# Performance work log

Measured on AMD Instinct MI355X. Metric: run time of the kernel, lower is better.

The kernel has to match this reference:

```python
import jax, jax.numpy as jnp
import numpy as np

HEADS = 4
DIM_HEAD = 32
GROUPS = 32  # min(256//4, 32)
EPS = 1e-5


def setup_inputs() -> dict:
    key = jax.random.key(0)
    ks = jax.random.split(key, 5)
    B, C, H, W = 16, 256, 64, 64
    CD, HC, WC = 512, 32, 32
    hid = HEADS * DIM_HEAD  # 128
    return {
        "x": jax.random.normal(ks[0], (B, C, H, W), jnp.float32),
        "cond": jax.random.normal(ks[1], (B, CD, HC, WC), jnp.float32),
        "gn_w": jnp.ones((C,), jnp.float32),
        "gn_b": jnp.zeros((C,), jnp.float32),
        "w_q": jax.random.normal(ks[2], (hid, C), jnp.float32) * 0.05,
        "b_q": jnp.zeros((hid,), jnp.float32),
        "w_kv": jax.random.normal(ks[3], (2 * hid, CD), jnp.float32) * 0.05,
        "b_kv": jnp.zeros((2 * hid,), jnp.float32),
        "w_out": jax.random.normal(ks[4], (C, hid), jnp.float32) * 0.05,
        "b_out": jnp.zeros((C,), jnp.float32),
    }


def _group_norm(x, w, b):
    # x: (B, C, H, W); normalize per group over (channels-in-group, H, W)
    B, C, H, W = x.shape
    xg = x.reshape(B, GROUPS, C // GROUPS, H, W)
    mu = jnp.mean(xg, axis=(2, 3, 4), keepdims=True)
    var = jnp.var(xg, axis=(2, 3, 4), keepdims=True)
    xn = ((xg - mu) * jax.lax.rsqrt(var + EPS)).reshape(B, C, H, W)
    return xn * w[None, :, None, None] + b[None, :, None, None]


def _conv1x1(x, w, b):
    # x: (B, Cin, H, W), w: (Cout, Cin), b: (Cout,)
    return jnp.einsum('oc,bchw->bohw', w, x) + b[None, :, None, None]


def reference(x, cond, gn_w, gn_b, w_q, b_q, w_kv, b_kv, w_out, b_out):
    B, C, H, W = x.shape
    hid = HEADS * DIM_HEAD
    xn = _group_norm(x, gn_w, gn_b)
    q = _conv1x1(xn, w_q, b_q)          # (B, hid, H, W)
    kv = _conv1x1(cond, w_kv, b_kv)     # (B, 2*hid, Hc, Wc)
    Nc = kv.shape[2] * kv.shape[3]
    N = H * W
    k = kv[:, :hid].reshape(B, HEADS, DIM_HEAD, Nc)
    v = kv[:, hid:].reshape(B, HEADS, DIM_HEAD, Nc)
    q = q.reshape(B, HEADS, DIM_HEAD, N)
    k = jax.nn.softmax(k, axis=-1)
    # kv outer product: (B, heads, d, e)
    context = jnp.einsum('bhdn,bhen->bhde', k, v)
    # query contraction over d: (B, heads, e, n)
    out = jnp.einsum('bhde,bhdn->bhen', context, q)
    out = out.reshape(B, hid, H, W)
    return _conv1x1(out, w_out, b_out)
```

## Files before the change

kernel.cpp:

```cpp
#include <hip/hip_runtime.h>
#include <hip/hip_bf16.h>

typedef __attribute__((ext_vector_type(8))) short bf16x8;
typedef __attribute__((ext_vector_type(4))) float f32x4;

__device__ __forceinline__ ushort f2bf(float f) {
    __hip_bfloat16 h = __float2bfloat16(f);
    return __builtin_bit_cast(ushort, h);
}
__device__ __forceinline__ unsigned pack2(float a, float b) {
    return (unsigned)f2bf(a) | ((unsigned)f2bf(b) << 16);
}
__device__ __forceinline__ float bflo(unsigned u) { return __uint_as_float(u << 16); }
__device__ __forceinline__ float bfhi(unsigned u) { return __uint_as_float(u & 0xffff0000u); }

__device__ __forceinline__ void unpack8(uint4 r, float* o) {
    o[0] = bflo(r.x); o[1] = bfhi(r.x); o[2] = bflo(r.y); o[3] = bfhi(r.y);
    o[4] = bflo(r.z); o[5] = bfhi(r.z); o[6] = bflo(r.w); o[7] = bfhi(r.w);
}

__global__ __launch_bounds__(256) void kvprep_kernel(const float* __restrict__ w_kv,
                                                     const float* __restrict__ cond,
                                                     const float* __restrict__ b_kv,
                                                     ushort* __restrict__ kv16,
                                                     const float* __restrict__ x,
                                                     float* __restrict__ statacc,
                                                     float* __restrict__ zbase) {
    __shared__ ushort lA[128 * 64];
    __shared__ ushort lB[64 * 64];
    __shared__ float scratch[64 * 64];
    __shared__ float red[8];
    int bid = blockIdx.x, t = threadIdx.x;
    if (bid < 512) {
        int nb = bid & 15, ob = (bid >> 4) & 1, b = bid >> 5;
        int col0 = nb * 64, row0 = ob * 128;
        int l = t & 63, wid = t >> 6;
        int wr = wid >> 1, wc = wid & 1;
        int lr = l & 15, lg = l >> 4;
        const float* Ab32 = w_kv + (size_t)row0 * 512;
        const float* Bb = cond + (size_t)b * 512 * 1024 + col0;
        int sp = t & 31, sj = t >> 5;
        int rA = t >> 3, gAr = t & 7, gw = gAr ^ (rA & 7);
        int rB = t >> 4, gB = t & 15;
        float4 ka0_, ka1_, ka2_, ka3_, ka4_, ka5_, ka6_, ka7_;
        float4 kb0_, kb1_, kb2_, kb3_;
#define KP_LOADA(k0) { \
    ka0_ = *(const float4*)&Ab32[(size_t)(rA)      * 512 + (k0) + gAr * 8]; \
    ka1_ = *(const float4*)&Ab32[(size_t)(rA)      * 512 + (k0) + gAr * 8 + 4]; \
    ka2_ = *(const float4*)&Ab32[(size_t)(32 + rA) * 512 + (k0) + gAr * 8]; \
    ka3_ = *(const float4*)&Ab32[(size_t)(32 + rA) * 512 + (k0) + gAr * 8 + 4]; \
    ka4_ = *(const float4*)&Ab32[(size_t)(64 + rA) * 512 + (k0) + gAr * 8]; \
    ka5_ = *(const float4*)&Ab32[(size_t)(64 + rA) * 512 + (k0) + gAr * 8 + 4]; \
    ka6_ = *(const float4*)&Ab32[(size_t)(96 + rA) * 512 + (k0) + gAr * 8]; \
    ka7_ = *(const float4*)&Ab32[(size_t)(96 + rA) * 512 + (k0) + gAr * 8 + 4]; }
#define KP_LOADB(k0) { \
    kb0_ = *(const float4*)&Bb[(size_t)((k0) + rB)      * 1024 + gB * 4]; \
    kb1_ = *(const float4*)&Bb[(size_t)((k0) + 16 + rB) * 1024 + gB * 4]; \
    kb2_ = *(const float4*)&Bb[(size_t)((k0) + 32 + rB) * 1024 + gB * 4]; \
    kb3_ = *(const float4*)&Bb[(size_t)((k0) + 48 + rB) * 1024 + gB * 4]; }
#define KP_WRITEA() { \
    uint4 p; \
    p.x = pack2(ka0_.x, ka0_.y); p.y = pack2(ka0_.z, ka0_.w); \
    p.z = pack2(ka1_.x, ka1_.y); p.w = pack2(ka1_.z, ka1_.w); \
    *(uint4*)((char*)lA + (size_t)((rA)      * 8 + gw) * 16) = p; \
    p.x = pack2(ka2_.x, ka2_.y); p.y = pack2(ka2_.z, ka2_.w); \
    p.z = pack2(ka3_.x, ka3_.y); p.w = pack2(ka3_.z, ka3_.w); \
    *(uint4*)((char*)lA + (size_t)((32 + rA) * 8 + gw) * 16) = p; \
    p.x = pack2(ka4_.x, ka4_.y); p.y = pack2(ka4_.z, ka4_.w); \
    p.z = pack2(ka5_.x, ka5_.y); p.w = pack2(ka5_.z, ka5_.w); \
    *(uint4*)((char*)lA + (size_t)((64 + rA) * 8 + gw) * 16) = p; \
    p.x = pack2(ka6_.x, ka6_.y); p.y = pack2(ka6_.z, ka6_.w); \
    p.z = pack2(ka7_.x, ka7_.y); p.w = pack2(ka7_.z, ka7_.w); \
    *(uint4*)((char*)lA + (size_t)((96 + rA) * 8 + gw) * 16) = p; }
#define KP_WRITEB() { \
    *(float4*)((char*)scratch + (rB)      * 256 + (gB ^ (((rB)      >> 1) & 15)) * 16) = kb0_; \
    *(float4*)((char*)scratch + (16 + rB) * 256 + (gB ^ (((16 + rB) >> 1) & 15)) * 16) = kb1_; \
    *(float4*)((char*)scratch + (32 + rB) * 256 + (gB ^ (((32 + rB) >> 1) & 15)) * 16) = kb2_; \
    *(float4*)((char*)scratch + (48 + rB) * 256 + (gB ^ (((48 + rB) >> 1) & 15)) * 16) = kb3_; }
#define KP_PACKB() { \
    int swz = sp & 15; \
    float4 s0 = *(const float4*)((char*)scratch + (2*sp)   * 256 + ((2*sj)   ^ swz) * 16); \
    float4 s1 = *(const float4*)((char*)scratch + (2*sp)   * 256 + ((2*sj+1) ^ swz) * 16); \
    float4 s2 = *(const float4*)((char*)scratch + (2*sp+1) * 256 + ((2*sj)   ^ swz) * 16); \
    float4 s3 = *(const float4*)((char*)scratch + (2*sp+1) * 256 + ((2*sj+1) ^ swz) * 16); \
    float c0v[8] = {s0.x, s0.y, s0.z, s0.w, s1.x, s1.y, s1.z, s1.w}; \
    float c1v[8] = {s2.x, s2.y, s2.z, s2.w, s3.x, s3.y, s3.z, s3.w}; \
    _Pragma("unroll") \
    for (int w = 0; w < 8; ++w) { \
        int n = sj * 8 + w; \
        unsigned pk = pack2(c0v[w], c1v[w]); \
        *(unsigned*)((char*)lB + n * 128 + (((sp >> 2) ^ (n & 7)) * 16) + (sp & 3) * 4) = pk; \
    } }
        KP_LOADA(0); KP_LOADB(0);
        f32x4 acc[4][2] = {};
        for (int it = 0; it < 8; ++it) {
            KP_WRITEA();
            KP_WRITEB();
            __syncthreads();
            if (it < 7) { KP_LOADA(it * 64 + 64); KP_LOADB(it * 64 + 64); }
            KP_PACKB();
            __syncthreads();
            #pragma unroll
            for (int ks = 0; ks < 2; ++ks) {
                bf16x8 av[4], bv[2];
                #pragma unroll
                for (int mi = 0; mi < 4; ++mi) {
                    int ar = wr * 64 + mi * 16 + lr;
                    int q = (ks * 4 + lg) ^ (ar & 7);
                    av[mi] = *(const bf16x8*)((const char*)lA + ar * 128 + q * 16);
                }
                #pragma unroll
                for (int ni = 0; ni < 2; ++ni) {
                    int br = wc * 32 + ni * 16 + lr;
                    int q = (ks * 4 + lg) ^ (br & 7);
                    bv[ni] = *(const bf16x8*)((const char*)lB + br * 128 + q * 16);
                }
                #pragma unroll
                for (int mi = 0; mi < 4; ++mi)
                    #pragma unroll
                    for (int ni = 0; ni < 2; ++ni)
                        acc[mi][ni] = __builtin_amdgcn_mfma_f32_16x16x32_bf16(
                            av[mi], bv[ni], acc[mi][ni], 0, 0, 0);
            }
            __syncthreads();
        }
#undef KP_LOADA
#undef KP_LOADB
#undef KP_WRITEA
#undef KP_WRITEB
#undef KP_PACKB
        int orow = row0 + wr * 64, ocol = col0 + wc * 32 + lr;
        #pragma unroll
        for (int mi = 0; mi < 4; ++mi) {
            int rb = orow + mi * 16 + lg * 4;
            float4 b4 = *(const float4*)&b_kv[rb];
            float bvr[4] = {b4.x, b4.y, b4.z, b4.w};
            #pragma unroll
            for (int ni = 0; ni < 2; ++ni) {
                int cc = ocol + ni * 16;
                #pragma unroll
                for (int r = 0; r < 4; ++r)
                    kv16[((size_t)b * 256 + rb + r) * 1024 + cc] = f2bf(acc[mi][ni][r] + bvr[r]);
            }
        }
    } else {
        int bg = bid - 512;
        int zi = bg * 256 + t;
        if (zi < 67584) zbase[zi] = 0.f;
        const float4* xp = (const float4*)(x + (size_t)bg * 32768);
        float s = 0.f, ss = 0.f;
        #pragma unroll
        for (int j = 0; j < 32; ++j) {
            float4 v = xp[t + 256 * j];
            s  += v.x + v.y + v.z + v.w;
            ss += v.x*v.x + v.y*v.y + v.z*v.z + v.w*v.w;
        }
        #pragma unroll
        for (int off = 32; off > 0; off >>= 1) {
            s  += __shfl_down(s, off, 64);
            ss += __shfl_down(ss, off, 64);
        }
        int wave = t >> 6;
        if ((t & 63) == 0) { red[wave * 2] = s; red[wave * 2 + 1] = ss; }
        __syncthreads();
        if (t == 0) {
            statacc[bg * 2]     = red[0] + red[2] + red[4] + red[6];
            statacc[bg * 2 + 1] = red[1] + red[3] + red[5] + red[7];
        }
    }
}

__global__ __launch_bounds__(256) void ctx_partial_kernel(const ushort* __restrict__ kv,
                                                          float* __restrict__ rowsum,
                                                          float* __restrict__ ctx) {
    int bh = blockIdx.y, b = bh >> 2, h = bh & 3;
    int n0 = blockIdx.x * 128;
    __shared__ float pl[32][129], vl[32][129];
    int t = threadIdx.x;
    int r = t >> 3, cs = (t & 7) * 16;
    const ushort* kp = kv + ((size_t)b * 256 + h * 32 + r) * 1024 + n0 + cs;
    const ushort* vp = kv + ((size_t)b * 256 + 128 + h * 32 + r) * 1024 + n0 + cs;
    float kvals[16], vvals[16];
    unpack8(((const uint4*)kp)[0], kvals);
    unpack8(((const uint4*)kp)[1], kvals + 8);
    unpack8(((const uint4*)vp)[0], vvals);
    unpack8(((const uint4*)vp)[1], vvals + 8);
    float psum = 0.f;
    #pragma unroll
    for (int i = 0; i < 16; ++i) {
        float e = __expf(kvals[i]);
        pl[r][cs + i] = e;
        vl[r][cs + i] = vvals[i];
        psum += e;
    }
    psum += __shfl_xor(psum, 1, 64);
    psum += __shfl_xor(psum, 2, 64);
    psum += __shfl_xor(psum, 4, 64);
    if ((t & 7) == 0) atomicAdd(&rowsum[bh * 32 + r], psum);
    __syncthreads();
    int d0 = t >> 5, e0 = t & 31;
    float acc[4] = {0.f, 0.f, 0.f, 0.f};
    #pragma unroll 8
    for (int nn = 0; nn < 128; ++nn) {
        float vv = vl[e0][nn];
        #pragma unroll
        for (int i = 0; i < 4; ++i)
            acc[i] += pl[d0 + 8 * i][nn] * vv;
    }
    #pragma unroll
    for (int i = 0; i < 4; ++i)
        atomicAdd(&ctx[((size_t)bh * 32 + d0 + 8 * i) * 32 + e0], acc[i]);
}

__global__ __launch_bounds__(256) void a_kernel(const float* __restrict__ ctx,
                                                const float* __restrict__ rowsum,
                                                const float* __restrict__ w_out,
                                                const float* __restrict__ w_q,
                                                const float* __restrict__ b_q,
                                                const float* __restrict__ statacc,
                                                const float* __restrict__ gn_w,
                                                const float* __restrict__ gn_b,
                                                const float* __restrict__ b_out,
                                                ushort* __restrict__ A16,
                                                float* __restrict__ biasb) {
    __shared__ float ctxl[4][32][33];
    __shared__ float wol[16][128];
    __shared__ float ml[16][128];
    __shared__ float cbuf[256][17];
    __shared__ float pbuf[16][17];
    int b = blockIdx.x >> 4, ot = (blockIdx.x & 15) << 4;
    int t = threadIdx.x;
    #pragma unroll
    for (int j = 0; j < 16; ++j) {
        int e = t + 256 * j;
        float inv = 1.f / rowsum[b * 128 + (e >> 5)];
        ctxl[e >> 10][(e >> 5) & 31][e & 31] = ctx[(size_t)b * 4096 + e] * inv;
    }
    #pragma unroll
    for (int j = 0; j < 8; ++j) {
        int e = t + 256 * j;
        wol[e >> 7][e & 127] = w_out[(ot + (e >> 7)) * 128 + (e & 127)];
    }
    __syncthreads();
    #pragma unroll
    for (int j = 0; j < 8; ++j) {
        int e = t + 256 * j;
        int o = e >> 7, hd = e & 127, h = hd >> 5, d = hd & 31;
        float acc = 0.f;
        #pragma unroll
        for (int ee = 0; ee < 32; ++ee) acc += wol[o][h * 32 + ee] * ctxl[h][d][ee];
        ml[o][hd] = acc;
    }
    __syncthreads();
    int c = t, g = c >> 3;
    float a0 = statacc[(b * 32 + g) * 2], a1 = statacc[(b * 32 + g) * 2 + 1];
    float mu  = a0 * (1.f / 32768.f);
    float var = a1 * (1.f / 32768.f) - mu * mu;
    float sc = rsqrtf(var + 1e-5f) * gn_w[c];
    float tc = gn_b[c] - mu * sc;
    float wt[16];
    #pragma unroll
    for (int o = 0; o < 16; ++o) wt[o] = 0.f;
    for (int hd = 0; hd < 128; ++hd) {
        float wq = w_q[hd * 256 + c];
        #pragma unroll
        for (int o = 0; o < 16; ++o) wt[o] += ml[o][hd] * wq;
    }
    ushort* Abp = A16 + ((size_t)b * 256 + ot) * 256 + c;
    #pragma unroll
    for (int o = 0; o < 16; ++o) {
        Abp[(size_t)o * 256] = f2bf(wt[o] * sc);
        cbuf[c][o] = wt[o] * tc;
    }
    __syncthreads();
    {
        int o = t >> 4, seg = t & 15;
        float p = 0.f;
        #pragma unroll
        for (int i = 0; i < 16; ++i) p += cbuf[seg * 16 + i][o];
        pbuf[o][seg] = p;
    }
    __syncthreads();
    if (t < 16) {
        int o = t;
        float sum = 0.f;
        #pragma unroll
        for (int s2 = 0; s2 < 16; ++s2) sum += pbuf[o][s2];
        float md = 0.f;
        #pragma unroll 8
        for (int hd = 0; hd < 128; ++hd) md += ml[o][hd] * b_q[hd];
        biasb[(size_t)b * 256 + ot + o] = sum + md + b_out[ot + o];
    }
}

__global__ __launch_bounds__(512) void out_gemm_fused(const ushort* __restrict__ A16,
                                                      const float* __restrict__ x,
                                                      const float* __restrict__ biasb,
                                                      float* __restrict__ out) {
    __shared__ ushort lA[256 * 64];
    __shared__ ushort lB[128 * 64];
    __shared__ float scratch[64 * 128];
    int b = blockIdx.y;
    int n0 = blockIdx.x * 128;
    int t = threadIdx.x;
    int l = t & 63, wid = t >> 6;
    int wr = wid >> 1, wc = wid & 1;
    int lr = l & 15, lg = l >> 4;
    const ushort* Ab = A16 + (size_t)b * 65536;
    const float* xb = x + (size_t)b * 256 * 4096 + n0;
    int sp = t & 31, sj = t >> 5;
    uint4 a0_, a1_, a2_, a3_;
    float4 b0_, b1_, b2_, b3_;
    int rA = t >> 3, gA = (t & 7) ^ (rA & 7);
    int rB = t >> 5, gB = t & 31;
#define OG_LOADA(k0) { \
    a0_ = *(const uint4*)(Ab + (size_t)(rA)       * 256 + (k0) + gA * 8); \
    a1_ = *(const uint4*)(Ab + (size_t)(64 + rA)  * 256 + (k0) + gA * 8); \
    a2_ = *(const uint4*)(Ab + (size_t)(128 + rA) * 256 + (k0) + gA * 8); \
    a3_ = *(const uint4*)(Ab + (size_t)(192 + rA) * 256 + (k0) + gA * 8); }
#define OG_LOADB(k0) { \
    b0_ = *(const float4*)&xb[(size_t)((k0) + rB)      * 4096 + gB * 4]; \
    b1_ = *(const float4*)&xb[(size_t)((k0) + 16 + rB) * 4096 + gB * 4]; \
    b2_ = *(const float4*)&xb[(size_t)((k0) + 32 + rB) * 4096 + gB * 4]; \
    b3_ = *(const float4*)&xb[(size_t)((k0) + 48 + rB) * 4096 + gB * 4]; }
    OG_LOADA(0); OG_LOADB(0);
    f32x4 acc[4][4] = {};
    for (int it = 0; it < 4; ++it) {
        *(uint4*)((char*)lA + (size_t)t * 16)          = a0_;
        *(uint4*)((char*)lA + (size_t)(512 + t) * 16)  = a1_;
        *(uint4*)((char*)lA + (size_t)(1024 + t) * 16) = a2_;
        *(uint4*)((char*)lA + (size_t)(1536 + t) * 16) = a3_;
        *(float4*)((char*)scratch + (rB)      * 512 + (gB ^ (((rB)      >> 1) & 31)) * 16) = b0_;
        *(float4*)((char*)scratch + (16 + rB) * 512 + (gB ^ (((16 + rB) >> 1) & 31)) * 16) = b1_;
        *(float4*)((char*)scratch + (32 + rB) * 512 + (gB ^ (((32 + rB) >> 1) & 31)) * 16) = b2_;
        *(float4*)((char*)scratch + (48 + rB) * 512 + (gB ^ (((48 + rB) >> 1) & 31)) * 16) = b3_;
        __syncthreads();
        if (it < 3) { OG_LOADA(it * 64 + 64); OG_LOADB(it * 64 + 64); }
        {
            int swz = sp & 31;
            float4 s0 = *(const float4*)((char*)scratch + (2*sp)   * 512 + ((2*sj)   ^ swz) * 16);
            float4 s1 = *(const float4*)((char*)scratch + (2*sp)   * 512 + ((2*sj+1) ^ swz) * 16);
            float4 s2 = *(const float4*)((char*)scratch + (2*sp+1) * 512 + ((2*sj)   ^ swz) * 16);
            float4 s3 = *(const float4*)((char*)scratch + (2*sp+1) * 512 + ((2*sj+1) ^ swz) * 16);
            float c0v[8] = {s0.x, s0.y, s0.z, s0.w, s1.x, s1.y, s1.z, s1.w};
            float c1v[8] = {s2.x, s2.y, s2.z, s2.w, s3.x, s3.y, s3.z, s3.w};
            #pragma unroll
            for (int w = 0; w < 8; ++w) {
                int n = sj * 8 + w;
                unsigned pk = pack2(c0v[w], c1v[w]);
                *(unsigned*)((char*)lB + n * 128 + (((sp >> 2) ^ (n & 7)) * 16) + (sp & 3) * 4) = pk;
            }
        }
        __syncthreads();
        #pragma unroll
        for (int ks = 0; ks < 2; ++ks) {
            bf16x8 av[4], bv[4];
            #pragma unroll
            for (int mi = 0; mi < 4; ++mi) {
                int ar = wr * 64 + mi * 16 + lr;
                int q = (ks * 4 + lg) ^ (ar & 7);
                av[mi] = *(const bf16x8*)((const char*)lA + ar * 128 + q * 16);
            }
            #pragma unroll
            for (int ni = 0; ni < 4; ++ni) {
                int br = wc * 64 + ni * 16 + lr;
                int q = (ks * 4 + lg) ^ (br & 7);
                bv[ni] = *(const bf16x8*)((const char*)lB + br * 128 + q * 16);
            }
            #pragma unroll
            for (int mi = 0; mi < 4; ++mi)
                #pragma unroll
                for (int ni = 0; ni < 4; ++ni)
                    acc[mi][ni] = __builtin_amdgcn_mfma_f32_16x16x32_bf16(
                        av[mi], bv[ni], acc[mi][ni], 0, 0, 0);
        }
        __syncthreads();
    }
#undef OG_LOADA
#undef OG_LOADB
    const float* bp = biasb + (size_t)b * 256;
    int orow = wr * 64, ocol = n0 + wc * 64 + lr;
    #pragma unroll
    for (int mi = 0; mi < 4; ++mi) {
        int rb = orow + mi * 16 + lg * 4;
        float4 b4 = *(const float4*)&bp[rb];
        float bvr[4] = {b4.x, b4.y, b4.z, b4.w};
        #pragma unroll
        for (int ni = 0; ni < 4; ++ni) {
            int cc = ocol + ni * 16;
            #pragma unroll
            for (int r = 0; r < 4; ++r)
                out[((size_t)b * 256 + rb + r) * 4096 + cc] = acc[mi][ni][r] + bvr[r];
        }
    }
}

extern "C" void kernel_launch(void* const* d_in, const int* in_sizes, int n_in,
                              void* d_out, int out_size, void* d_ws, size_t ws_size,
                              hipStream_t stream) {
    const float* x     = (const float*)d_in[0];
    const float* cond  = (const float*)d_in[1];
    const float* gn_w  = (const float*)d_in[2];
    const float* gn_b  = (const float*)d_in[3];
    const float* w_q   = (const float*)d_in[4];
    const float* b_q   = (const float*)d_in[5];
    const float* w_kv  = (const float*)d_in[6];
    const float* b_kv  = (const float*)d_in[7];
    const float* w_out = (const float*)d_in[8];
    const float* b_out = (const float*)d_in[9];
    float* out = (float*)d_out;

    float* f       = (float*)d_ws;
    float* statacc = f;
    float* rowsum  = f + 1024;
    float* ctx     = f + 3072;
    float* biasb   = f + 68608;
    ushort* u      = (ushort*)(f + 72704);
    ushort* kv16   = u;
    ushort* A16    = u + 4194304;

    kvprep_kernel<<<1024, 256, 0, stream>>>(w_kv, cond, b_kv, kv16, x, statacc, rowsum);
    ctx_partial_kernel<<<dim3(8, 64), 256, 0, stream>>>(kv16, rowsum, ctx);
    a_kernel<<<256, 256, 0, stream>>>(ctx, rowsum, w_out, w_q, b_q, statacc,
                                      gn_w, gn_b, b_out, A16, biasb);
    out_gemm_fused<<<dim3(32, 16), 512, 0, stream>>>(A16, x, biasb, out);
}
```

Measured before the change: 80.67 us.

## Fuse KV projection, softmax exp and context outer product into one kernel

After: 77.89 us. 1.04x faster.

```diff
diff --git a/kernel.cpp b/kernel.cpp
--- a/kernel.cpp
+++ b/kernel.cpp
@@ -12,146 +12,190 @@
     return (unsigned)f2bf(a) | ((unsigned)f2bf(b) << 16);
 }
 __device__ __forceinline__ float bflo(unsigned u) { return __uint_as_float(u << 16); }
-__device__ __forceinline__ float bfhi(unsigned u) { return __uint_as_float(u & 0xffff0000u); }
-
-__device__ __forceinline__ void unpack8(uint4 r, float* o) {
-    o[0] = bflo(r.x); o[1] = bfhi(r.x); o[2] = bflo(r.y); o[3] = bfhi(r.y);
-    o[4] = bflo(r.z); o[5] = bfhi(r.z); o[6] = bflo(r.w); o[7] = bfhi(r.w);
-}
-
-__global__ __launch_bounds__(256) void kvprep_kernel(const float* __restrict__ w_kv,
-                                                     const float* __restrict__ cond,
-                                                     const float* __restrict__ b_kv,
-                                                     ushort* __restrict__ kv16,
-                                                     const float* __restrict__ x,
-                                                     float* __restrict__ statacc,
-                                                     float* __restrict__ zbase) {
-    __shared__ ushort lA[128 * 64];
+
+__global__ __launch_bounds__(512) void kvctx_kernel(const float* __restrict__ w_kv,
+                                                    const float* __restrict__ cond,
+                                                    const float* __restrict__ b_kv,
+                                                    const float* __restrict__ x,
+                                                    float* __restrict__ statacc,
+                                                    float* __restrict__ rsp,
+                                                    float* __restrict__ ctxp) {
+    __shared__ ushort lA[256 * 64];
     __shared__ ushort lB[64 * 64];
     __shared__ float scratch[64 * 64];
-    __shared__ float red[8];
+    __shared__ float red[16];
     int bid = blockIdx.x, t = threadIdx.x;
-    if (bid < 512) {
-        int nb = bid & 15, ob = (bid >> 4) & 1, b = bid >> 5;
-        int col0 = nb * 64, row0 = ob * 128;
-        int l = t & 63, wid = t >> 6;
-        int wr = wid >> 1, wc = wid & 1;
+    if (bid < 256) {
+        int b = bid >> 4, nc = bid & 15;
+        int col0 = nc * 64;
+        int l = t & 63, w = t >> 6;
         int lr = l & 15, lg = l >> 4;
-        const float* Ab32 = w_kv + (size_t)row0 * 512;
         const float* Bb = cond + (size_t)b * 512 * 1024 + col0;
-        int sp = t & 31, sj = t >> 5;
         int rA = t >> 3, gAr = t & 7, gw = gAr ^ (rA & 7);
         int rB = t >> 4, gB = t & 15;
+        int sp = t & 31, sj4 = t >> 5;
         float4 ka0_, ka1_, ka2_, ka3_, ka4_, ka5_, ka6_, ka7_;
-        float4 kb0_, kb1_, kb2_, kb3_;
-#define KP_LOADA(k0) { \
-    ka0_ = *(const float4*)&Ab32[(size_t)(rA)      * 512 + (k0) + gAr * 8]; \
-    ka1_ = *(const float4*)&Ab32[(size_t)(rA)      * 512 + (k0) + gAr * 8 + 4]; \
-    ka2_ = *(const float4*)&Ab32[(size_t)(32 + rA) * 512 + (k0) + gAr * 8]; \
-    ka3_ = *(const float4*)&Ab32[(size_t)(32 + rA) * 512 + (k0) + gAr * 8 + 4]; \
-    ka4_ = *(const float4*)&Ab32[(size_t)(64 + rA) * 512 + (k0) + gAr * 8]; \
-    ka5_ = *(const float4*)&Ab32[(size_t)(64 + rA) * 512 + (k0) + gAr * 8 + 4]; \
-    ka6_ = *(const float4*)&Ab32[(size_t)(96 + rA) * 512 + (k0) + gAr * 8]; \
-    ka7_ = *(const float4*)&Ab32[(size_t)(96 + rA) * 512 + (k0) + gAr * 8 + 4]; }
-#define KP_LOADB(k0) { \
+        float4 kb0_, kb1_;
+#define KC_LOADA(k0) { \
+    ka0_ = *(const float4*)&w_kv[(size_t)(rA)       * 512 + (k0) + gAr * 8]; \
+    ka1_ = *(const float4*)&w_kv[(size_t)(rA)       * 512 + (k0) + gAr * 8 + 4]; \
+    ka2_ = *(const float4*)&w_kv[(size_t)(64 + rA)  * 512 + (k0) + gAr * 8]; \
+    ka3_ = *(const float4*)&w_kv[(size_t)(64 + rA)  * 512 + (k0) + gAr * 8 + 4]; \
+    ka4_ = *(const float4*)&w_kv[(size_t)(128 + rA) * 512 + (k0) + gAr * 8]; \
+    ka5_ = *(const float4*)&w_kv[(size_t)(128 + rA) * 512 + (k0) + gAr * 8 + 4]; \
+    ka6_ = *(const float4*)&w_kv[(size_t)(192 + rA) * 512 + (k0) + gAr * 8]; \
+    ka7_ = *(const float4*)&w_kv[(size_t)(192 + rA) * 512 + (k0) + gAr * 8 + 4]; }
+#define KC_LOADB(k0) { \
     kb0_ = *(const float4*)&Bb[(size_t)((k0) + rB)      * 1024 + gB * 4]; \
-    kb1_ = *(const float4*)&Bb[(size_t)((k0) + 16 + rB) * 1024 + gB * 4]; \
-    kb2_ = *(const float4*)&Bb[(size_t)((k0) + 32 + rB) * 1024 + gB * 4]; \
-    kb3_ = *(const float4*)&Bb[(size_t)((k0) + 48 + rB) * 1024 + gB * 4]; }
-#define KP_WRITEA() { \
-    uint4 p; \
+    kb1_ = *(const float4*)&Bb[(size_t)((k0) + 32 + rB) * 1024 + gB * 4]; }
+#define KC_WRITEA() { uint4 p; \
     p.x = pack2(ka0_.x, ka0_.y); p.y = pack2(ka0_.z, ka0_.w); \
     p.z = pack2(ka1_.x, ka1_.y); p.w = pack2(ka1_.z, ka1_.w); \
-    *(uint4*)((char*)lA + (size_t)((rA)      * 8 + gw) * 16) = p; \
+    *(uint4*)((char*)lA + (size_t)((rA)       * 8 + gw) * 16) = p; \
     p.x = pack2(ka2_.x, ka2_.y); p.y = pack2(ka2_.z, ka2_.w); \
     p.z = pack2(ka3_.x, ka3_.y); p.w = pack2(ka3_.z, ka3_.w); \
-    *(uint4*)((char*)lA + (size_t)((32 + rA) * 8 + gw) * 16) = p; \
+    *(uint4*)((char*)lA + (size_t)((64 + rA)  * 8 + gw) * 16) = p; \
     p.x = pack2(ka4_.x, ka4_.y); p.y = pack2(ka4_.z, ka4_.w); \
     p.z = pack2(ka5_.x, ka5_.y); p.w = pack2(ka5_.z, ka5_.w); \
-    *(uint4*)((char*)lA + (size_t)((64 + rA) * 8 + gw) * 16) = p; \
+    *(uint4*)((char*)lA + (size_t)((128 + rA) * 8 + gw) * 16) = p; \
     p.x = pack2(ka6_.x, ka6_.y); p.y = pack2(ka6_.z, ka6_.w); \
     p.z = pack2(ka7_.x, ka7_.y); p.w = pack2(ka7_.z, ka7_.w); \
-    *(uint4*)((char*)lA + (size_t)((96 + rA) * 8 + gw) * 16) = p; }
-#define KP_WRITEB() { \
-    *(float4*)((char*)scratch + (rB)      * 256 + (gB ^ (((rB)      >> 1) & 15)) * 16) = kb0_; \
-    *(float4*)((char*)scratch + (16 + rB) * 256 + (gB ^ (((16 + rB) >> 1) & 15)) * 16) = kb1_; \
-    *(float4*)((char*)scratch + (32 + rB) * 256 + (gB ^ (((32 + rB) >> 1) & 15)) * 16) = kb2_; \
-    *(float4*)((char*)scratch + (48 + rB) * 256 + (gB ^ (((48 + rB) >> 1) & 15)) * 16) = kb3_; }
-#define KP_PACKB() { \
+    *(uint4*)((char*)lA + (size_t)((192 + rA) * 8 + gw) * 16) = p; }
+#define KC_WRITEB() { \
+    *(float4*)((char*)scratch + (rB)      * 256 + ((gB ^ (((rB)      >> 1) & 15)) * 16)) = kb0_; \
+    *(float4*)((char*)scratch + (32 + rB) * 256 + ((gB ^ (((32 + rB) >> 1) & 15)) * 16)) = kb1_; }
+#define KC_PACKB() { \
     int swz = sp & 15; \
-    float4 s0 = *(const float4*)((char*)scratch + (2*sp)   * 256 + ((2*sj)   ^ swz) * 16); \
-    float4 s1 = *(const float4*)((char*)scratch + (2*sp)   * 256 + ((2*sj+1) ^ swz) * 16); \
-    float4 s2 = *(const float4*)((char*)scratch + (2*sp+1) * 256 + ((2*sj)   ^ swz) * 16); \
-    float4 s3 = *(const float4*)((char*)scratch + (2*sp+1) * 256 + ((2*sj+1) ^ swz) * 16); \
-    float c0v[8] = {s0.x, s0.y, s0.z, s0.w, s1.x, s1.y, s1.z, s1.w}; \
-    float c1v[8] = {s2.x, s2.y, s2.z, s2.w, s3.x, s3.y, s3.z, s3.w}; \
+    float4 s0 = *(const float4*)((char*)scratch + (2*sp)   * 256 + ((sj4 ^ swz) * 16)); \
+    float4 s2 = *(const float4*)((char*)scratch + (2*sp+1) * 256 + ((sj4 ^ swz) * 16)); \
+    float c0v[4] = {s0.x, s0.y, s0.z, s0.w}; \
+    float c1v[4] = {s2.x, s2.y, s2.z, s2.w}; \
     _Pragma("unroll") \
-    for (int w = 0; w < 8; ++w) { \
-        int n = sj * 8 + w; \
-        unsigned pk = pack2(c0v[w], c1v[w]); \
+    for (int w4 = 0; w4 < 4; ++w4) { \
+        int n = sj4 * 4 + w4; \
+        unsigned pk = pack2(c0v[w4], c1v[w4]); \
         *(unsigned*)((char*)lB + n * 128 + (((sp >> 2) ^ (n & 7)) * 16) + (sp & 3) * 4) = pk; \
     } }
-        KP_LOADA(0); KP_LOADB(0);
-        f32x4 acc[4][2] = {};
+        KC_LOADA(0); KC_LOADB(0);
+        f32x4 acc[2][4] = {};
         for (int it = 0; it < 8; ++it) {
-            KP_WRITEA();
-            KP_WRITEB();
+            KC_WRITEA();
+            KC_WRITEB();
             __syncthreads();
-            if (it < 7) { KP_LOADA(it * 64 + 64); KP_LOADB(it * 64 + 64); }
-            KP_PACKB();
+            if (it < 7) { KC_LOADA(it * 64 + 64); KC_LOADB(it * 64 + 64); }
+            KC_PACKB();
             __syncthreads();
             #pragma unroll
             for (int ks = 0; ks < 2; ++ks) {
-                bf16x8 av[4], bv[2];
-                #pragma unroll
-                for (int mi = 0; mi < 4; ++mi) {
-                    int ar = wr * 64 + mi * 16 + lr;
+                bf16x8 av[2], bv[4];
+                #pragma unroll
+                for (int mi = 0; mi < 2; ++mi) {
+                    int ar = w * 32 + mi * 16 + lr;
                     int q = (ks * 4 + lg) ^ (ar & 7);
                     av[mi] = *(const bf16x8*)((const char*)lA + ar * 128 + q * 16);
                 }
                 #pragma unroll
-                for (int ni = 0; ni < 2; ++ni) {
-                    int br = wc * 32 + ni * 16 + lr;
+                for (int ni = 0; ni < 4; ++ni) {
+                    int br = ni * 16 + lr;
                     int q = (ks * 4 + lg) ^ (br & 7);
                     bv[ni] = *(const bf16x8*)((const char*)lB + br * 128 + q * 16);
                 }
                 #pragma unroll
-                for (int mi = 0; mi < 4; ++mi)
+                for (int mi = 0; mi < 2; ++mi)
                     #pragma unroll
-                    for (int ni = 0; ni < 2; ++ni)
+                    for (int ni = 0; ni < 4; ++ni)
                         acc[mi][ni] = __builtin_amdgcn_mfma_f32_16x16x32_bf16(
                             av[mi], bv[ni], acc[mi][ni], 0, 0, 0);
             }
             __syncthreads();
         }
-#undef KP_LOADA
-#undef KP_LOADB
-#undef KP_WRITEA
-#undef KP_WRITEB
-#undef KP_PACKB
-        int orow = row0 + wr * 64, ocol = col0 + wc * 32 + lr;
-        #pragma unroll
-        for (int mi = 0; mi < 4; ++mi) {
-            int rb = orow + mi * 16 + lg * 4;
-            float4 b4 = *(const float4*)&b_kv[rb];
-            float bvr[4] = {b4.x, b4.y, b4.z, b4.w};
-            #pragma unroll
-            for (int ni = 0; ni < 2; ++ni) {
-                int cc = ocol + ni * 16;
-                #pragma unroll
-                for (int r = 0; r < 4; ++r)
-                    kv16[((size_t)b * 256 + rb + r) * 1024 + cc] = f2bf(acc[mi][ni][r] + bvr[r]);
+#undef KC_LOADA
+#undef KC_LOADB
+#undef KC_WRITEA
+#undef KC_WRITEB
+#undef KC_PACKB
+        bool isK = (w < 4);
+        float bk[2][4];
+        #pragma unroll
+        for (int mi = 0; mi < 2; ++mi)
+            #pragma unroll
+            for (int reg = 0; reg < 4; ++reg)
+                bk[mi][reg] = b_kv[w * 32 + mi * 16 + lg * 4 + reg];
+        float rs[2][4];
+        #pragma unroll
+        for (int mi = 0; mi < 2; ++mi)
+            #pragma unroll
+            for (int reg = 0; reg < 4; ++reg) rs[mi][reg] = 0.f;
+        #pragma unroll
+        for (int mi = 0; mi < 2; ++mi) {
+            #pragma unroll
+            for (int ni = 0; ni < 4; ++ni) {
+                #pragma unroll
+                for (int reg = 0; reg < 4; ++reg) {
+                    int R = w * 32 + mi * 16 + lg * 4 + reg;
+                    int N = ni * 16 + lr;
+                    float val = acc[mi][ni][reg] + bk[mi][reg];
+                    ushort uo;
+                    if (isK) {
+                        uo = f2bf(__expf(val));
+                        rs[mi][reg] += bflo((unsigned)uo);
+                    } else {
+                        uo = f2bf(val);
+                    }
+                    *(ushort*)((char*)lA + R * 128 + (((N >> 3) ^ (R & 7)) * 16) + (N & 7) * 2) = uo;
+                }
+            }
+        }
+        if (isK) {
+            #pragma unroll
+            for (int mi = 0; mi < 2; ++mi) {
+                #pragma unroll
+                for (int reg = 0; reg < 4; ++reg) {
+                    float v = rs[mi][reg];
+                    v += __shfl_xor(v, 1, 64);
+                    v += __shfl_xor(v, 2, 64);
+                    v += __shfl_xor(v, 4, 64);
+                    v += __shfl_xor(v, 8, 64);
+                    if (lr == 0)
+                        rsp[(size_t)(b * 16 + nc) * 128 + w * 32 + mi * 16 + lg * 4 + reg] = v;
+                }
+            }
+        }
+        __syncthreads();
+        if (isK) {
+            f32x4 c00 = {}, c01 = {}, c10 = {}, c11 = {};
+            #pragma unroll
+            for (int ks = 0; ks < 2; ++ks) {
+                int ar0 = w * 32 + lr,        qa0 = (ks * 4 + lg) ^ (ar0 & 7);
+                int ar1 = w * 32 + 16 + lr,   qa1 = (ks * 4 + lg) ^ (ar1 & 7);
+                int br0 = 128 + w * 32 + lr,      qb0 = (ks * 4 + lg) ^ (br0 & 7);
+                int br1 = 128 + w * 32 + 16 + lr, qb1 = (ks * 4 + lg) ^ (br1 & 7);
+                bf16x8 pa0 = *(const bf16x8*)((const char*)lA + ar0 * 128 + qa0 * 16);
+                bf16x8 pa1 = *(const bf16x8*)((const char*)lA + ar1 * 128 + qa1 * 16);
+                bf16x8 pv0 = *(const bf16x8*)((const char*)lA + br0 * 128 + qb0 * 16);
+                bf16x8 pv1 = *(const bf16x8*)((const char*)lA + br1 * 128 + qb1 * 16);
+                c00 = __builtin_amdgcn_mfma_f32_16x16x32_bf16(pa0, pv0, c00, 0, 0, 0);
+                c01 = __builtin_amdgcn_mfma_f32_16x16x32_bf16(pa0, pv1, c01, 0, 0, 0);
+                c10 = __builtin_amdgcn_mfma_f32_16x16x32_bf16(pa1, pv0, c10, 0, 0, 0);
+                c11 = __builtin_amdgcn_mfma_f32_16x16x32_bf16(pa1, pv1, c11, 0, 0, 0);
+            }
+            float* cp = ctxp + (size_t)(b * 16 + nc) * 4096 + w * 1024;
+            #pragma unroll
+            for (int reg = 0; reg < 4; ++reg) {
+                int d0 = lg * 4 + reg;
+                cp[d0 * 32 + lr]              = c00[reg];
+                cp[d0 * 32 + 16 + lr]         = c01[reg];
+                cp[(16 + d0) * 32 + lr]       = c10[reg];
+                cp[(16 + d0) * 32 + 16 + lr]  = c11[reg];
             }
         }
     } else {
-        int bg = bid - 512;
-        int zi = bg * 256 + t;
-        if (zi < 67584) zbase[zi] = 0.f;
+        int bg = bid - 256;
         const float4* xp = (const float4*)(x + (size_t)bg * 32768);
         float s = 0.f, ss = 0.f;
         #pragma unroll
-        for (int j = 0; j < 32; ++j) {
-            float4 v = xp[t + 256 * j];
+        for (int j = 0; j < 16; ++j) {
+            float4 v = xp[t + 512 * j];
             s  += v.x + v.y + v.z + v.w;
             ss += v.x*v.x + v.y*v.y + v.z*v.z + v.w*v.w;
         }
@@ -164,56 +208,17 @@
         if ((t & 63) == 0) { red[wave * 2] = s; red[wave * 2 + 1] = ss; }
         __syncthreads();
         if (t == 0) {
-            statacc[bg * 2]     = red[0] + red[2] + red[4] + red[6];
-            statacc[bg * 2 + 1] = red[1] + red[3] + red[5] + red[7];
-        }
-    }
-}
-
-__global__ __launch_bounds__(256) void ctx_partial_kernel(const ushort* __restrict__ kv,
-                                                          float* __restrict__ rowsum,
-                                                          float* __restrict__ ctx) {
-    int bh = blockIdx.y, b = bh >> 2, h = bh & 3;
-    int n0 = blockIdx.x * 128;
-    __shared__ float pl[32][129], vl[32][129];
-    int t = threadIdx.x;
-    int r = t >> 3, cs = (t & 7) * 16;
-    const ushort* kp = kv + ((size_t)b * 256 + h * 32 + r) * 1024 + n0 + cs;
-    const ushort* vp = kv + ((size_t)b * 256 + 128 + h * 32 + r) * 1024 + n0 + cs;
-    float kvals[16], vvals[16];
-    unpack8(((const uint4*)kp)[0], kvals);
-    unpack8(((const uint4*)kp)[1], kvals + 8);
-    unpack8(((const uint4*)vp)[0], vvals);
-    unpack8(((const uint4*)vp)[1], vvals + 8);
-    float psum = 0.f;
-    #pragma unroll
-    for (int i = 0; i < 16; ++i) {
-        float e = __expf(kvals[i]);
-        pl[r][cs + i] = e;
-        vl[r][cs + i] = vvals[i];
-        psum += e;
-    }
-    psum += __shfl_xor(psum, 1, 64);
-    psum += __shfl_xor(psum, 2, 64);
-    psum += __shfl_xor(psum, 4, 64);
-    if ((t & 7) == 0) atomicAdd(&rowsum[bh * 32 + r], psum);
-    __syncthreads();
-    int d0 = t >> 5, e0 = t & 31;
-    float acc[4] = {0.f, 0.f, 0.f, 0.f};
-    #pragma unroll 8
-    for (int nn = 0; nn < 128; ++nn) {
-        float vv = vl[e0][nn];
-        #pragma unroll
-        for (int i = 0; i < 4; ++i)
-            acc[i] += pl[d0 + 8 * i][nn] * vv;
-    }
-    #pragma unroll
-    for (int i = 0; i < 4; ++i)
-        atomicAdd(&ctx[((size_t)bh * 32 + d0 + 8 * i) * 32 + e0], acc[i]);
-}
-
-__global__ __launch_bounds__(256) void a_kernel(const float* __restrict__ ctx,
-                                                const float* __restrict__ rowsum,
+            float S = 0.f, SS = 0.f;
+            #pragma unroll
+            for (int i = 0; i < 8; ++i) { S += red[i * 2]; SS += red[i * 2 + 1]; }
+            statacc[bg * 2]     = S;
+            statacc[bg * 2 + 1] = SS;
+        }
+    }
+}
+
+__global__ __launch_bounds__(256) void a_kernel(const float* __restrict__ ctxp,
+                                                const float* __restrict__ rsp,
                                                 const float* __restrict__ w_out,
                                                 const float* __restrict__ w_q,
                                                 const float* __restrict__ b_q,
@@ -228,18 +233,30 @@
     __shared__ float ml[16][128];
     __shared__ float cbuf[256][17];
     __shared__ float pbuf[16][17];
+    __shared__ float rsinv[128];
     int b = blockIdx.x >> 4, ot = (blockIdx.x & 15) << 4;
     int t = threadIdx.x;
-    #pragma unroll
-    for (int j = 0; j < 16; ++j) {
-        int e = t + 256 * j;
-        float inv = 1.f / rowsum[b * 128 + (e >> 5)];
-        ctxl[e >> 10][(e >> 5) & 31][e & 31] = ctx[(size_t)b * 4096 + e] * inv;
+    if (t < 128) {
+        float s = 0.f;
+        #pragma unroll
+        for (int nc = 0; nc < 16; ++nc)
+            s += rsp[(size_t)(b * 16 + nc) * 128 + t];
+        rsinv[t] = 1.f / s;
     }
     #pragma unroll
     for (int j = 0; j < 8; ++j) {
         int e = t + 256 * j;
         wol[e >> 7][e & 127] = w_out[(ot + (e >> 7)) * 128 + (e & 127)];
+    }
+    __syncthreads();
+    #pragma unroll
+    for (int j = 0; j < 16; ++j) {
+        int e = t + 256 * j;
+        float v = 0.f;
+        #pragma unroll
+        for (int nc = 0; nc < 16; ++nc)
+            v += ctxp[(size_t)(b * 16 + nc) * 4096 + e];
+        ctxl[e >> 10][(e >> 5) & 31][e & 31] = v * rsinv[e >> 5];
     }
     __syncthreads();
     #pragma unroll
@@ -412,16 +429,13 @@
 
     float* f       = (float*)d_ws;
     float* statacc = f;
-    float* rowsum  = f + 1024;
-    float* ctx     = f + 3072;
-    float* biasb   = f + 68608;
-    ushort* u      = (ushort*)(f + 72704);
-    ushort* kv16   = u;
-    ushort* A16    = u + 4194304;
-
-    kvprep_kernel<<<1024, 256, 0, stream>>>(w_kv, cond, b_kv, kv16, x, statacc, rowsum);
-    ctx_partial_kernel<<<dim3(8, 64), 256, 0, stream>>>(kv16, rowsum, ctx);
-    a_kernel<<<256, 256, 0, stream>>>(ctx, rowsum, w_out, w_q, b_q, statacc,
+    float* rsp     = f + 1024;
+    float* ctxp    = f + 33792;
+    float* biasb   = f + 1082368;
+    ushort* A16    = (ushort*)(f + 1086464);
+
+    kvctx_kernel<<<768, 512, 0, stream>>>(w_kv, cond, b_kv, x, statacc, rsp, ctxp);
+    a_kernel<<<256, 256, 0, stream>>>(ctxp, rsp, w_out, w_q, b_q, statacc,
                                       gn_w, gn_b, b_out, A16, biasb);
     out_gemm_fused<<<dim3(32, 16), 512, 0, stream>>>(A16, x, biasb, out);
 }
```
